# Kernel tuning notes

Measured on AMD Instinct MI355X. Metric: run time of the kernel, lower is better.

## Reference

```python
import jax, jax.numpy as jnp
import numpy as np

# --- static config (from init_kwargs) ---
B = 256        # num graphs
NPG = 128      # nodes per graph
EPG = 512      # edges per graph
DIN = 128      # dim_node
D = 256        # dim_hidden
RATIO = 0.5    # causal_ratio
N_RES = int(RATIO * EPG)
BN_EPS = 1e-5


def setup_inputs() -> dict:
    key = jax.random.key(0)
    ks = jax.random.split(key, 24)
    N = B * NPG
    x = jax.random.normal(ks[0], (N, DIN), jnp.float32)
    # edges confined within each graph, contiguous per graph (graph-sorted)
    src = jax.random.randint(ks[1], (B, EPG), 0, NPG)
    dst = jax.random.randint(ks[2], (B, EPG), 0, NPG)
    off = (jnp.arange(B, dtype=jnp.int32) * NPG)[:, None]
    edge_index = jnp.stack([(src + off).reshape(-1), (dst + off).reshape(-1)], 0).astype(jnp.int32)
    batch = jnp.repeat(jnp.arange(B, dtype=jnp.int32), NPG)

    s = 0.05
    def rn(k, shape):
        return jax.random.normal(k, shape, jnp.float32) * s
    p = dict(
        x=x, edge_index=edge_index, batch=batch,
        vemb=rn(ks[3], (1, D)),
        # conv1 GIN mlp: Linear(DIN,2D) -> BN -> ReLU -> Linear(2D,D)
        W1a=rn(ks[4], (DIN, 2 * D)), b1a=jnp.zeros((2 * D,)),
        g1a=jnp.ones((2 * D,)), be1a=jnp.zeros((2 * D,)),
        W1b=rn(ks[5], (2 * D, D)), b1b=jnp.zeros((D,)),
        g1=jnp.ones((D,)), be1=jnp.zeros((D,)),          # outer batch_norm1
        # conv2 GIN mlp
        W2a=rn(ks[6], (D, 2 * D)), b2a=jnp.zeros((2 * D,)),
        g2a=jnp.ones((2 * D,)), be2a=jnp.zeros((2 * D,)),
        W2b=rn(ks[7], (2 * D, D)), b2b=jnp.zeros((D,)),
        g2=jnp.ones((D,)), be2=jnp.zeros((D,)),          # outer batch_norm2
        # edge scorer: Linear(2D, 1)
        Wl=rn(ks[8], (2 * D, 1)), bl=jnp.zeros((1,)),
    )
    return p


def _bn(h, g, b):
    mu = h.mean(0)
    var = jnp.mean((h - mu) ** 2, 0)
    return (h - mu) * jax.lax.rsqrt(var + BN_EPS) * g + b


def reference(x, edge_index, batch, vemb,
              W1a, b1a, g1a, be1a, W1b, b1b, g1, be1,
              W2a, b2a, g2a, be2a, W2b, b2b, g2, be2,
              Wl, bl):
    N = x.shape[0]
    row, col = edge_index[0], edge_index[1]

    def gin(h, Wa, ba, ga, bta, Wb, bb):
        # GINConv, eps=0: mlp(h + sum_{j->i} h_j), aggregate src feats at dst
        agg = jax.ops.segment_sum(h[row], col, num_segments=N)
        z = (h + agg) @ Wa + ba
        z = jax.nn.relu(_bn(z, ga, bta))
        return z @ Wb + bb

    # layer 1: conv1 -> bn -> relu (dropout_rate = 0)
    post = jax.nn.relu(_bn(gin(x, W1a, b1a, g1a, be1a, W1b, b1b), g1, be1))
    # virtual node gather (embedding of index 0, one per graph)
    vfeat = jnp.broadcast_to(vemb[0], (B, D))
    post = post + vfeat[batch]
    # layer 2 (last): conv2 -> bn, no relu
    xn = _bn(gin(post, W2a, b2a, g2a, be2a, W2b, b2b), g2, be2)

    # edge scoring
    erep = jnp.concatenate([xn[row], xn[col]], axis=-1)          # [E, 2D]
    pred = (erep @ Wl + bl.astype(erep.dtype)).reshape(-1)       # [E]

    # per-graph top-k split (equal EPG edges per graph)
    pw = pred.reshape(B, EPG)
    order = jnp.argsort(-pw, axis=1)
    idx_r, idx_d = order[:, :N_RES], order[:, N_RES:]
    causal_w = jnp.take_along_axis(pw, idx_r, 1).reshape(-1)
    conf_w = -jnp.take_along_axis(pw, idx_d, 1).reshape(-1)
    ei = edge_index.reshape(2, B, EPG)
    causal_ei = jnp.take_along_axis(ei, jnp.broadcast_to(idx_r[None], (2, B, N_RES)), axis=2).reshape(2, -1)
    conf_ei = jnp.take_along_axis(ei, jnp.broadcast_to(idx_d[None], (2, B, EPG - N_RES)), axis=2).reshape(2, -1)
    return (causal_ei, causal_w, conf_ei, conf_w, pred)
```

## Files before the change

### kernel.cpp

```cpp
#include <hip/hip_runtime.h>

#define BGR   256
#define NPG   128
#define EPG   512
#define DIN   128
#define DD    256
#define DD2   512
#define NTOT  (BGR * NPG)
#define ETOT  (BGR * EPG)
#define NRES  (EPG / 2)
#define NCHUNK 256
#define MP    136

#define OFF_CEI  0
#define OFF_CW   (2 * BGR * NRES)
#define OFF_FEI  (OFF_CW + BGR * NRES)
#define OFF_FW   (OFF_FEI + 2 * BGR * NRES)
#define OFF_PRED (OFF_FW + BGR * NRES)

typedef unsigned short ushortt;
typedef __attribute__((ext_vector_type(4))) unsigned short us4;
typedef __attribute__((ext_vector_type(8))) unsigned short us8;
typedef __attribute__((ext_vector_type(8))) short short8;
typedef __attribute__((ext_vector_type(4))) float f32x4;

__device__ __forceinline__ ushortt f2bf(float f) {
    unsigned int u = __float_as_uint(f);
    unsigned int r = (u + 0x7fffu + ((u >> 16) & 1u)) >> 16;
    return (ushortt)r;
}
__device__ __forceinline__ float bf2f(ushortt u) {
    return __uint_as_float(((unsigned int)u) << 16);
}

__device__ __forceinline__ void g2lds16(const void* g, void* l) {
    __builtin_amdgcn_global_load_lds(
        (const __attribute__((address_space(1))) unsigned int*)g,
        (__attribute__((address_space(3))) unsigned int*)l, 16, 0, 0);
}

__global__ __launch_bounds__(256) void convert_all(const float* __restrict__ W1a,
                                                   const float* __restrict__ W1b,
                                                   const float* __restrict__ W2a,
                                                   const float* __restrict__ W2b,
                                                   ushortt* __restrict__ Wt1a,
                                                   ushortt* __restrict__ Wt1b,
                                                   ushortt* __restrict__ Wt2a,
                                                   ushortt* __restrict__ Wt2b) {
    const int idx = blockIdx.x * 256 + threadIdx.x;
    if (idx < 65536) {
        const int k = idx >> 9, n = idx & 511;
        Wt1a[n * DIN + k] = f2bf(W1a[idx]);
    } else if (idx < 196608) {
        const int i = idx - 65536;
        const int k = i >> 8, n = i & 255;
        Wt1b[n * DD2 + k] = f2bf(W1b[i]);
    } else if (idx < 327680) {
        const int i = idx - 196608;
        const int k = i >> 9, n = i & 511;
        Wt2a[n * DD + k] = f2bf(W2a[i]);
    } else if (idx < 458752) {
        const int i = idx - 327680;
        const int k = i >> 8, n = i & 255;
        Wt2b[n * DD2 + k] = f2bf(W2b[i]);
    }
}

__global__ __launch_bounds__(256) void build_adj(const int* __restrict__ ei,
                                                 ushortt* __restrict__ Madj) {
    __shared__ int cnt[NPG * NPG];
    const int b = blockIdx.x, t = threadIdx.x;
    for (int i = t; i < NPG * NPG; i += 256) cnt[i] = 0;
    __syncthreads();
    for (int e = t; e < EPG; e += 256) {
        const int src = ei[b * EPG + e] - b * NPG;
        const int dst = ei[ETOT + b * EPG + e] - b * NPG;
        atomicAdd(&cnt[dst * NPG + src], 1);
    }
    __syncthreads();
#pragma unroll
    for (int k = 0; k < 8; ++k) {
        const int i0 = (t + k * 256) * 8;
        us8 o;
#pragma unroll
        for (int e = 0; e < 8; ++e) {
            const int i = i0 + e;
            const int v = cnt[i] + (((i >> 7) == (i & 127)) ? 1 : 0);
            o[e] = f2bf((float)v);
        }
        *(us8*)&Madj[(size_t)b * NPG * NPG + i0] = o;
    }
}

__global__ __launch_bounds__(256) void agg1_mm(const float* __restrict__ x,
                                               const ushortt* __restrict__ Madj,
                                               ushortt* __restrict__ s1) {
    __shared__ ushortt Ms[NPG * MP];
    __shared__ ushortt XT[DIN * MP];
    const int b = blockIdx.x, t = threadIdx.x;
    const int wave = t >> 6, lane = t & 63;
    const int qd = lane >> 4, r = lane & 15;
    const ushortt* Mg = Madj + (size_t)b * NPG * NPG;
#pragma unroll
    for (int k = 0; k < 8; ++k) {
        const int ch = t + k * 256;
        const int m = ch >> 4, sc = (ch & 15) * 8;
        *(us8*)&Ms[m * MP + sc] = *(const us8*)&Mg[m * NPG + sc];
    }
#pragma unroll 4
    for (int it = 0; it < 64; ++it) {
        const int s = it * 2 + (t >> 7);
        const int c = t & 127;
        XT[c * MP + s] = f2bf(x[(size_t)(b * NPG + s) * DIN + c]);
    }
    __syncthreads();
    const int wm = (wave >> 1) * 64, wn = (wave & 1) * 64;
    f32x4 acc[4][4] = {};
#pragma unroll
    for (int ks = 0; ks < 4; ++ks) {
        const int k0 = ks * 32 + qd * 8;
        short8 af[4], bfr[4];
#pragma unroll
        for (int i = 0; i < 4; ++i)
            af[i] = *(const short8*)&Ms[(wm + i * 16 + r) * MP + k0];
#pragma unroll
        for (int j = 0; j < 4; ++j)
            bfr[j] = *(const short8*)&XT[(wn + j * 16 + r) * MP + k0];
#pragma unroll
        for (int i = 0; i < 4; ++i)
#pragma unroll
            for (int j = 0; j < 4; ++j)
                acc[i][j] = __builtin_amdgcn_mfma_f32_16x16x32_bf16(af[i], bfr[j], acc[i][j], 0, 0, 0);
    }
    __syncthreads();
    ushortt* Cs = Ms;
#pragma unroll
    for (int j = 0; j < 4; ++j) {
        const int coll = wn + j * 16 + r;
#pragma unroll
        for (int i = 0; i < 4; ++i)
#pragma unroll
            for (int tt = 0; tt < 4; ++tt)
                Cs[(wm + i * 16 + qd * 4 + tt) * DIN + coll] = f2bf(acc[i][j][tt]);
    }
    __syncthreads();
#pragma unroll
    for (int k = 0; k < 8; ++k) {
        const int ch = t + k * 256;
        const int row = ch >> 4, colc = (ch & 15) * 8;
        *(us8*)&s1[(size_t)(b * NPG + row) * DIN + colc] = *(const us8*)&Cs[row * DIN + colc];
    }
}

__global__ __launch_bounds__(256) void agg2_mm(const ushortt* __restrict__ h,
                                               const float* __restrict__ scale,
                                               const float* __restrict__ shift,
                                               const float* __restrict__ vemb,
                                               const ushortt* __restrict__ Madj,
                                               ushortt* __restrict__ s2) {
    __shared__ ushortt Ms[NPG * MP];
    __shared__ ushortt PT[NPG * MP];
    const int nb = blockIdx.x, b = blockIdx.y, t = threadIdx.x;
    const int wave = t >> 6, lane = t & 63;
    const int qd = lane >> 4, r = lane & 15;
    const ushortt* Mg = Madj + (size_t)b * NPG * NPG;
#pragma unroll
    for (int k = 0; k < 8; ++k) {
        const int ch = t + k * 256;
        const int m = ch >> 4, sc = (ch & 15) * 8;
        *(us8*)&Ms[m * MP + sc] = *(const us8*)&Mg[m * NPG + sc];
    }
    const int cl = t & 127;
    const int c = nb * 128 + cl;
    const float scv = scale[c], shv = shift[c], vev = vemb[c];
#pragma unroll 4
    for (int it = 0; it < 64; ++it) {
        const int s = it * 2 + (t >> 7);
        float v = fmaf(bf2f(h[(size_t)(b * NPG + s) * DD + c]), scv, shv);
        PT[cl * MP + s] = f2bf(fmaxf(v, 0.0f) + vev);
    }
    __syncthreads();
    const int wm = (wave >> 1) * 64, wn = (wave & 1) * 64;
    f32x4 acc[4][4] = {};
#pragma unroll
    for (int ks = 0; ks < 4; ++ks) {
        const int k0 = ks * 32 + qd * 8;
        short8 af[4], bfr[4];
#pragma unroll
        for (int i = 0; i < 4; ++i)
            af[i] = *(const short8*)&Ms[(wm + i * 16 + r) * MP + k0];
#pragma unroll
        for (int j = 0; j < 4; ++j)
            bfr[j] = *(const short8*)&PT[(wn + j * 16 + r) * MP + k0];
#pragma unroll
        for (int i = 0; i < 4; ++i)
#pragma unroll
            for (int j = 0; j < 4; ++j)
                acc[i][j] = __builtin_amdgcn_mfma_f32_16x16x32_bf16(af[i], bfr[j], acc[i][j], 0, 0, 0);
    }
    __syncthreads();
    ushortt* Cs = Ms;
#pragma unroll
    for (int j = 0; j < 4; ++j) {
        const int coll = wn + j * 16 + r;
#pragma unroll
        for (int i = 0; i < 4; ++i)
#pragma unroll
            for (int tt = 0; tt < 4; ++tt)
                Cs[(wm + i * 16 + qd * 4 + tt) * 128 + coll] = f2bf(acc[i][j][tt]);
    }
    __syncthreads();
#pragma unroll
    for (int k = 0; k < 8; ++k) {
        const int ch = t + k * 256;
        const int row = ch >> 4, colc = (ch & 15) * 8;
        *(us8*)&s2[(size_t)(b * NPG + row) * DD + nb * 128 + colc] =
            *(const us8*)&Cs[row * 128 + colc];
    }
}

#define BM 128
#define BN 128
#define BK 32
__global__ __launch_bounds__(256) void gemm_mfma(const ushortt* __restrict__ A,
                                                 const ushortt* __restrict__ Wt,
                                                 const float* __restrict__ bias,
                                                 ushortt* __restrict__ C,
                                                 float* __restrict__ psum,
                                                 float* __restrict__ psumsq,
                                                 int M, int N, int K) {
    __shared__ ushortt As[BM * BK];
    __shared__ ushortt Bs[BN * BK];
    __shared__ ushortt Cs[BM * BN];
    __shared__ float redS[2][BN];
    __shared__ float redQ[2][BN];
    const int tid  = threadIdx.x;
    const int wave = tid >> 6;
    const int lane = tid & 63;
    const int qd = lane >> 4;
    const int r  = lane & 15;
    const int wm = (wave >> 1) * 64;
    const int wn = (wave & 1) * 64;
    const int m0 = blockIdx.y * BM;
    const int n0 = blockIdx.x * BN;

    f32x4 acc[4][4] = {};

    for (int k0 = 0; k0 < K; k0 += BK) {
#pragma unroll
        for (int s = 0; s < 2; ++s) {
            const int o   = wave * 128 + s * 64 + lane;
            const int row = o >> 2;
            const int cg  = o & 3;
            g2lds16(A  + (size_t)(m0 + row) * K + k0 + cg * 8,
                    &As[(size_t)(wave * 128 + s * 64) * 8]);
            g2lds16(Wt + (size_t)(n0 + row) * K + k0 + cg * 8,
                    &Bs[(size_t)(wave * 128 + s * 64) * 8]);
        }
        __syncthreads();
        short8 af[4], bfr[4];
#pragma unroll
        for (int i = 0; i < 4; ++i)
            af[i] = *(const short8*)&As[(wm + i * 16 + r) * BK + qd * 8];
#pragma unroll
        for (int j = 0; j < 4; ++j)
            bfr[j] = *(const short8*)&Bs[(wn + j * 16 + r) * BK + qd * 8];
#pragma unroll
        for (int i = 0; i < 4; ++i)
#pragma unroll
            for (int j = 0; j < 4; ++j)
                acc[i][j] = __builtin_amdgcn_mfma_f32_16x16x32_bf16(af[i], bfr[j], acc[i][j], 0, 0, 0);
        __syncthreads();
    }

#pragma unroll
    for (int j = 0; j < 4; ++j) {
        const int coll = wn + j * 16 + r;
        const float bv = bias[n0 + coll];
        float s = 0.0f, q = 0.0f;
#pragma unroll
        for (int i = 0; i < 4; ++i) {
#pragma unroll
            for (int t = 0; t < 4; ++t) {
                const float v = acc[i][j][t] + bv;
                Cs[(wm + i * 16 + qd * 4 + t) * BN + coll] = f2bf(v);
                s += v;
                q = fmaf(v, v, q);
            }
        }
        s += __shfl_xor(s, 16); s += __shfl_xor(s, 32);
        q += __shfl_xor(q, 16); q += __shfl_xor(q, 32);
        if (qd == 0) {
            redS[wave >> 1][coll] = s;
            redQ[wave >> 1][coll] = q;
        }
    }
    __syncthreads();
    if (tid < BN) {
        psum[(size_t)blockIdx.y * N + n0 + tid]   = redS[0][tid] + redS[1][tid];
        psumsq[(size_t)blockIdx.y * N + n0 + tid] = redQ[0][tid] + redQ[1][tid];
    }
#pragma unroll
    for (int s8 = 0; s8 < 8; ++s8) {
        const int c    = tid + 256 * s8;
        const int row  = c >> 4;
        const int colc = (c & 15) * 8;
        const us8 v = *(const us8*)&Cs[row * BN + colc];
        *(us8*)&C[(size_t)(m0 + row) * N + n0 + colc] = v;
    }
}

__global__ __launch_bounds__(256) void bn_finalize(const float* __restrict__ psum,
                                                   const float* __restrict__ psumsq,
                                                   const float* __restrict__ g,
                                                   const float* __restrict__ be,
                                                   int ncols,
                                                   float* __restrict__ scale,
                                                   float* __restrict__ shift) {
    const int c = blockIdx.x * 256 + threadIdx.x;
    double s = 0.0, s2 = 0.0;
    for (int k = 0; k < NCHUNK; ++k) {
        s += (double)psum[(size_t)k * ncols + c];
        s2 += (double)psumsq[(size_t)k * ncols + c];
    }
    const double mean = s / (double)NTOT;
    const double var = s2 / (double)NTOT - mean * mean;
    const double rs = 1.0 / sqrt(var + 1e-5);
    const float sc = (float)((double)g[c] * rs);
    scale[c] = sc;
    shift[c] = (float)((double)be[c] - mean * (double)sc);
}

__global__ __launch_bounds__(256) void bn_apply_vec(const ushortt* __restrict__ z,
                                                    const float* __restrict__ scale,
                                                    const float* __restrict__ shift,
                                                    ushortt* __restrict__ outp,
                                                    int ncolmask) {
    const size_t gi = (size_t)blockIdx.x * 256 + threadIdx.x;
    const size_t base = gi * 8;
    const int c0 = (int)(base & (size_t)ncolmask);
    const us8 z8 = *(const us8*)&z[base];
    us8 o;
#pragma unroll
    for (int e = 0; e < 8; ++e) {
        float v = fmaf(bf2f(z8[e]), scale[c0 + e], shift[c0 + e]);
        v = fmaxf(v, 0.0f);
        o[e] = f2bf(v);
    }
    *(us8*)&outp[base] = o;
}

__global__ __launch_bounds__(256) void node_dots_bn(const ushortt* __restrict__ h2,
                                                    const float* __restrict__ scale,
                                                    const float* __restrict__ shift,
                                                    const float* __restrict__ Wl,
                                                    float* __restrict__ pa,
                                                    float* __restrict__ pb) {
    const int wave = threadIdx.x >> 6;
    const int lane = threadIdx.x & 63;
    const int node = blockIdx.x * 4 + wave;
    const us4 z4 = *(const us4*)&h2[(size_t)node * DD + lane * 4];
    const float4 sc = *(const float4*)&scale[lane * 4];
    const float4 sh = *(const float4*)&shift[lane * 4];
    const float4 w0 = *(const float4*)&Wl[lane * 4];
    const float4 w1 = *(const float4*)&Wl[DD + lane * 4];
    const float x0 = fmaf(bf2f(z4.x), sc.x, sh.x);
    const float x1 = fmaf(bf2f(z4.y), sc.y, sh.y);
    const float x2 = fmaf(bf2f(z4.z), sc.z, sh.z);
    const float x3 = fmaf(bf2f(z4.w), sc.w, sh.w);
    float sa = x0 * w0.x + x1 * w0.y + x2 * w0.z + x3 * w0.w;
    float sb = x0 * w1.x + x1 * w1.y + x2 * w1.z + x3 * w1.w;
#pragma unroll
    for (int off = 32; off >= 1; off >>= 1) {
        sa += __shfl_down(sa, off);
        sb += __shfl_down(sb, off);
    }
    if (lane == 0) {
        pa[node] = sa;
        pb[node] = sb;
    }
}

__global__ __launch_bounds__(EPG) void sort_write(const float* __restrict__ pa,
                                                  const float* __restrict__ pb,
                                                  const float* __restrict__ bl,
                                                  const int* __restrict__ ei,
                                                  float* __restrict__ out) {
    __shared__ float pw[EPG];
    __shared__ int ord[EPG];
    const int b = blockIdx.x;
    const int t = threadIdx.x;
    const int rg = ei[b * EPG + t];
    const int cg = ei[ETOT + b * EPG + t];
    const float v = pa[rg] + pb[cg] + bl[0];
    pw[t] = v;
    out[OFF_PRED + b * EPG + t] = v;
    __syncthreads();
    int rank = 0;
#pragma unroll 8
    for (int k = 0; k < EPG; ++k) {
        const float u = pw[k];
        rank += (u > v) || (u == v && k < t);
    }
    ord[rank] = t;
    __syncthreads();
    const int j = ord[t];
    const float wv = pw[j];
    const float e0 = (float)ei[b * EPG + j];
    const float e1 = (float)ei[ETOT + b * EPG + j];
    if (t < NRES) {
        out[OFF_CEI + b * NRES + t] = e0;
        out[OFF_CEI + BGR * NRES + b * NRES + t] = e1;
        out[OFF_CW + b * NRES + t] = wv;
    } else {
        const int p = t - NRES;
        out[OFF_FEI + b * NRES + p] = e0;
        out[OFF_FEI + BGR * NRES + b * NRES + p] = e1;
        out[OFF_FW + b * NRES + p] = -wv;
    }
}

extern "C" void kernel_launch(void* const* d_in, const int* in_sizes, int n_in,
                              void* d_out, int out_size, void* d_ws, size_t ws_size,
                              hipStream_t stream) {
    (void)in_sizes; (void)n_in; (void)out_size; (void)ws_size;
    const float* x    = (const float*)d_in[0];
    const int*   ei   = (const int*)d_in[1];
    const float* vemb = (const float*)d_in[3];
    const float* W1a  = (const float*)d_in[4];
    const float* b1a  = (const float*)d_in[5];
    const float* g1a  = (const float*)d_in[6];
    const float* be1a = (const float*)d_in[7];
    const float* W1b  = (const float*)d_in[8];
    const float* b1b  = (const float*)d_in[9];
    const float* g1   = (const float*)d_in[10];
    const float* be1  = (const float*)d_in[11];
    const float* W2a  = (const float*)d_in[12];
    const float* b2a  = (const float*)d_in[13];
    const float* g2a  = (const float*)d_in[14];
    const float* be2a = (const float*)d_in[15];
    const float* W2b  = (const float*)d_in[16];
    const float* b2b  = (const float*)d_in[17];
    const float* g2   = (const float*)d_in[18];
    const float* be2  = (const float*)d_in[19];
    const float* Wl   = (const float*)d_in[20];
    const float* bl   = (const float*)d_in[21];
    float* out = (float*)d_out;

    char* wp = (char*)d_ws;
    auto alloc = [&](size_t bytes) -> char* {
        char* r = wp;
        wp += (bytes + 255) & ~(size_t)255;
        return r;
    };
    ushortt* zb    = (ushortt*)alloc((size_t)NTOT * 512 * 2);
    ushortt* bufC  = (ushortt*)alloc((size_t)NTOT * 512 * 2);
    ushortt* bufD  = (ushortt*)alloc((size_t)NTOT * 256 * 2);
    ushortt* bufS1 = (ushortt*)alloc((size_t)NTOT * 128 * 2);
    ushortt* Madj  = (ushortt*)alloc((size_t)BGR * NPG * NPG * 2);
    ushortt* Wt1a  = (ushortt*)alloc((size_t)DIN * DD2 * 2);
    ushortt* Wt1b  = (ushortt*)alloc((size_t)DD2 * DD * 2);
    ushortt* Wt2a  = (ushortt*)alloc((size_t)DD * DD2 * 2);
    ushortt* Wt2b  = (ushortt*)alloc((size_t)DD2 * DD * 2);
    float*   psum   = (float*)alloc((size_t)NCHUNK * 512 * 4);
    float*   psumsq = (float*)alloc((size_t)NCHUNK * 512 * 4);
    float*   scale  = (float*)alloc(512 * 4);
    float*   shift  = (float*)alloc(512 * 4);
    float*   pa     = (float*)alloc((size_t)NTOT * 4);
    float*   pb     = (float*)alloc((size_t)NTOT * 4);

    convert_all<<<1792, 256, 0, stream>>>(W1a, W1b, W2a, W2b, Wt1a, Wt1b, Wt2a, Wt2b);

    build_adj<<<BGR, 256, 0, stream>>>(ei, Madj);

    agg1_mm<<<BGR, 256, 0, stream>>>(x, Madj, bufS1);

    gemm_mfma<<<dim3(DD2 / BN, NTOT / BM), 256, 0, stream>>>(bufS1, Wt1a, b1a, zb, psum, psumsq, NTOT, DD2, DIN);
    bn_finalize<<<2, 256, 0, stream>>>(psum, psumsq, g1a, be1a, DD2, scale, shift);
    bn_apply_vec<<<(NTOT * DD2) / 2048, 256, 0, stream>>>(zb, scale, shift, bufC, DD2 - 1);

    gemm_mfma<<<dim3(DD / BN, NTOT / BM), 256, 0, stream>>>(bufC, Wt1b, b1b, zb, psum, psumsq, NTOT, DD, DD2);
    bn_finalize<<<1, 256, 0, stream>>>(psum, psumsq, g1, be1, DD, scale, shift);

    agg2_mm<<<dim3(2, BGR), 256, 0, stream>>>(zb, scale, shift, vemb, Madj, bufD);

    gemm_mfma<<<dim3(DD2 / BN, NTOT / BM), 256, 0, stream>>>(bufD, Wt2a, b2a, zb, psum, psumsq, NTOT, DD2, DD);
    bn_finalize<<<2, 256, 0, stream>>>(psum, psumsq, g2a, be2a, DD2, scale, shift);
    bn_apply_vec<<<(NTOT * DD2) / 2048, 256, 0, stream>>>(zb, scale, shift, bufC, DD2 - 1);

    gemm_mfma<<<dim3(DD / BN, NTOT / BM), 256, 0, stream>>>(bufC, Wt2b, b2b, zb, psum, psumsq, NTOT, DD, DD2);
    bn_finalize<<<1, 256, 0, stream>>>(psum, psumsq, g2, be2, DD, scale, shift);

    node_dots_bn<<<NTOT / 4, 256, 0, stream>>>(zb, scale, shift, Wl, pa, pb);

    sort_write<<<BGR, EPG, 0, stream>>>(pa, pb, bl, ei, out);
}
```

Measured before the change: 344.7 us.

## Fuse whole GIN pipeline into one cooperative persistent kernel with grid syncs

Replaces the sequence of many separate launches (weight convert, adjacency build, aggregations, four GEMMs, BN finalize/apply, dots, sort) with a single cooperative kernel of one 512-thread block per graph, keeping per-graph adjacency and hidden activations resident in about 146 KB of LDS and separating BN statistic phases with grid.sync. The aim is to remove launch overhead and the global round trips for intermediates like bufC, bufS1 and Madj. In exchange it depends on all 256 blocks being co-resident, adds many grid-wide barriers, and runs each GEMM as per-graph tiles that reload weights in every block.

After: 538.7 us. 56.3% more time.

```diff
diff --git a/kernel.cpp b/kernel.cpp
--- a/kernel.cpp
+++ b/kernel.cpp
@@ -1,4 +1,7 @@
 #include <hip/hip_runtime.h>
+#include <hip/hip_cooperative_groups.h>
+
+namespace cg = cooperative_groups;
 
 #define BGR   256
 #define NPG   128
@@ -9,8 +12,13 @@
 #define NTOT  (BGR * NPG)
 #define ETOT  (BGR * EPG)
 #define NRES  (EPG / 2)
-#define NCHUNK 256
 #define MP    136
+
+#define SM_A  0
+#define SM_H  34816
+#define SM_B  104448
+#define SM_S  141312
+#define SM_TOTAL 149504
 
 #define OFF_CEI  0
 #define OFF_CW   (2 * BGR * NRES)
@@ -19,7 +27,6 @@
 #define OFF_PRED (OFF_FW + BGR * NRES)
 
 typedef unsigned short ushortt;
-typedef __attribute__((ext_vector_type(4))) unsigned short us4;
 typedef __attribute__((ext_vector_type(8))) unsigned short us8;
 typedef __attribute__((ext_vector_type(8))) short short8;
 typedef __attribute__((ext_vector_type(4))) float f32x4;
@@ -32,391 +39,417 @@
 __device__ __forceinline__ float bf2f(ushortt u) {
     return __uint_as_float(((unsigned int)u) << 16);
 }
-
 __device__ __forceinline__ void g2lds16(const void* g, void* l) {
     __builtin_amdgcn_global_load_lds(
         (const __attribute__((address_space(1))) unsigned int*)g,
         (__attribute__((address_space(3))) unsigned int*)l, 16, 0, 0);
 }
 
-__global__ __launch_bounds__(256) void convert_all(const float* __restrict__ W1a,
-                                                   const float* __restrict__ W1b,
-                                                   const float* __restrict__ W2a,
-                                                   const float* __restrict__ W2b,
-                                                   ushortt* __restrict__ Wt1a,
-                                                   ushortt* __restrict__ Wt1b,
-                                                   ushortt* __restrict__ Wt2a,
-                                                   ushortt* __restrict__ Wt2b) {
-    const int idx = blockIdx.x * 256 + threadIdx.x;
-    if (idx < 65536) {
-        const int k = idx >> 9, n = idx & 511;
-        Wt1a[n * DIN + k] = f2bf(W1a[idx]);
-    } else if (idx < 196608) {
-        const int i = idx - 65536;
-        const int k = i >> 8, n = i & 255;
-        Wt1b[n * DD2 + k] = f2bf(W1b[i]);
-    } else if (idx < 327680) {
-        const int i = idx - 196608;
-        const int k = i >> 9, n = i & 511;
-        Wt2a[n * DD + k] = f2bf(W2a[i]);
-    } else if (idx < 458752) {
-        const int i = idx - 327680;
-        const int k = i >> 8, n = i & 255;
-        Wt2b[n * DD2 + k] = f2bf(W2b[i]);
-    }
-}
-
-__global__ __launch_bounds__(256) void build_adj(const int* __restrict__ ei,
-                                                 ushortt* __restrict__ Madj) {
-    __shared__ int cnt[NPG * NPG];
-    const int b = blockIdx.x, t = threadIdx.x;
-    for (int i = t; i < NPG * NPG; i += 256) cnt[i] = 0;
-    __syncthreads();
-    for (int e = t; e < EPG; e += 256) {
-        const int src = ei[b * EPG + e] - b * NPG;
-        const int dst = ei[ETOT + b * EPG + e] - b * NPG;
-        atomicAdd(&cnt[dst * NPG + src], 1);
-    }
-    __syncthreads();
-#pragma unroll
-    for (int k = 0; k < 8; ++k) {
-        const int i0 = (t + k * 256) * 8;
-        us8 o;
-#pragma unroll
-        for (int e = 0; e < 8; ++e) {
-            const int i = i0 + e;
-            const int v = cnt[i] + (((i >> 7) == (i & 127)) ? 1 : 0);
-            o[e] = f2bf((float)v);
-        }
-        *(us8*)&Madj[(size_t)b * NPG * NPG + i0] = o;
-    }
-}
-
-__global__ __launch_bounds__(256) void agg1_mm(const float* __restrict__ x,
-                                               const ushortt* __restrict__ Madj,
-                                               ushortt* __restrict__ s1) {
-    __shared__ ushortt Ms[NPG * MP];
-    __shared__ ushortt XT[DIN * MP];
-    const int b = blockIdx.x, t = threadIdx.x;
+__device__ __forceinline__ void mfma_tile_ld(const ushortt* Ap, const ushortt* Bp,
+                                             int wm, int wn, int qd, int r,
+                                             f32x4 acc[4][2]) {
+#pragma unroll
+    for (int ks = 0; ks < 4; ++ks) {
+        const int k0 = ks * 32 + qd * 8;
+        short8 af[4], bfr[2];
+#pragma unroll
+        for (int i = 0; i < 4; ++i)
+            af[i] = *(const short8*)&Ap[(wm + i * 16 + r) * MP + k0];
+#pragma unroll
+        for (int j = 0; j < 2; ++j)
+            bfr[j] = *(const short8*)&Bp[(wn + j * 16 + r) * MP + k0];
+#pragma unroll
+        for (int i = 0; i < 4; ++i)
+#pragma unroll
+            for (int j = 0; j < 2; ++j)
+                acc[i][j] = __builtin_amdgcn_mfma_f32_16x16x32_bf16(af[i], bfr[j], acc[i][j], 0, 0, 0);
+    }
+}
+
+__device__ __forceinline__ void scatter_rowmajor(ushortt* dst, f32x4 acc[4][2],
+                                                 int wm, int wn, int qd, int r) {
+#pragma unroll
+    for (int j = 0; j < 2; ++j) {
+        const int col = wn + j * 16 + r;
+#pragma unroll
+        for (int i = 0; i < 4; ++i)
+#pragma unroll
+            for (int tt = 0; tt < 4; ++tt)
+                dst[(wm + i * 16 + qd * 4 + tt) * MP + col] = f2bf(acc[i][j][tt]);
+    }
+}
+
+__device__ __forceinline__ void zgemm_phase(char* smem, int b, int t,
+                                            const ushortt* __restrict__ Wt, int wtStride, int khn,
+                                            const float* __restrict__ bias,
+                                            ushortt* __restrict__ zb,
+                                            float* __restrict__ psA, float* __restrict__ pqA) {
     const int wave = t >> 6, lane = t & 63;
     const int qd = lane >> 4, r = lane & 15;
-    const ushortt* Mg = Madj + (size_t)b * NPG * NPG;
-#pragma unroll
-    for (int k = 0; k < 8; ++k) {
-        const int ch = t + k * 256;
-        const int m = ch >> 4, sc = (ch & 15) * 8;
-        *(us8*)&Ms[m * MP + sc] = *(const us8*)&Mg[m * NPG + sc];
-    }
-#pragma unroll 4
-    for (int it = 0; it < 64; ++it) {
-        const int s = it * 2 + (t >> 7);
-        const int c = t & 127;
-        XT[c * MP + s] = f2bf(x[(size_t)(b * NPG + s) * DIN + c]);
-    }
-    __syncthreads();
-    const int wm = (wave >> 1) * 64, wn = (wave & 1) * 64;
-    f32x4 acc[4][4] = {};
-#pragma unroll
-    for (int ks = 0; ks < 4; ++ks) {
-        const int k0 = ks * 32 + qd * 8;
-        short8 af[4], bfr[4];
-#pragma unroll
-        for (int i = 0; i < 4; ++i)
-            af[i] = *(const short8*)&Ms[(wm + i * 16 + r) * MP + k0];
-#pragma unroll
-        for (int j = 0; j < 4; ++j)
-            bfr[j] = *(const short8*)&XT[(wn + j * 16 + r) * MP + k0];
-#pragma unroll
-        for (int i = 0; i < 4; ++i)
-#pragma unroll
-            for (int j = 0; j < 4; ++j)
-                acc[i][j] = __builtin_amdgcn_mfma_f32_16x16x32_bf16(af[i], bfr[j], acc[i][j], 0, 0, 0);
-    }
-    __syncthreads();
-    ushortt* Cs = Ms;
-#pragma unroll
-    for (int j = 0; j < 4; ++j) {
-        const int coll = wn + j * 16 + r;
-#pragma unroll
-        for (int i = 0; i < 4; ++i)
-#pragma unroll
-            for (int tt = 0; tt < 4; ++tt)
-                Cs[(wm + i * 16 + qd * 4 + tt) * DIN + coll] = f2bf(acc[i][j][tt]);
-    }
-    __syncthreads();
-#pragma unroll
-    for (int k = 0; k < 8; ++k) {
-        const int ch = t + k * 256;
-        const int row = ch >> 4, colc = (ch & 15) * 8;
-        *(us8*)&s1[(size_t)(b * NPG + row) * DIN + colc] = *(const us8*)&Cs[row * DIN + colc];
-    }
-}
-
-__global__ __launch_bounds__(256) void agg2_mm(const ushortt* __restrict__ h,
-                                               const float* __restrict__ scale,
-                                               const float* __restrict__ shift,
-                                               const float* __restrict__ vemb,
-                                               const ushortt* __restrict__ Madj,
-                                               ushortt* __restrict__ s2) {
-    __shared__ ushortt Ms[NPG * MP];
-    __shared__ ushortt PT[NPG * MP];
-    const int nb = blockIdx.x, b = blockIdx.y, t = threadIdx.x;
+    const int wm = (wave >> 2) * 64, wn = (wave & 3) * 32;
+    ushortt* Wc = (ushortt*)(smem + SM_B);
+    float* redS = (float*)(smem + SM_S + 4096);
+    float* redQ = (float*)(smem + SM_S + 5120);
+    for (int nc = 0; nc < 4; ++nc) {
+        f32x4 acc[4][2] = {};
+        for (int kh = 0; kh < khn; ++kh) {
+#pragma unroll
+            for (int kk = 0; kk < 4; ++kk) {
+                const int ch = t + kk * 512;
+                const int n = ch >> 4, k8 = (ch & 15) * 8;
+                *(us8*)&Wc[n * MP + k8] =
+                    *(const us8*)&Wt[(size_t)(nc * 128 + n) * wtStride + kh * 128 + k8];
+            }
+            __syncthreads();
+            const ushortt* Ap = (const ushortt*)(smem + SM_H) + kh * 17408;
+            mfma_tile_ld(Ap, Wc, wm, wn, qd, r, acc);
+            __syncthreads();
+        }
+        ushortt* Cs = Wc;
+#pragma unroll
+        for (int j = 0; j < 2; ++j) {
+            const int coll = wn + j * 16 + r;
+            const float bv = bias[nc * 128 + coll];
+            float s = 0.f, q = 0.f;
+#pragma unroll
+            for (int i = 0; i < 4; ++i)
+#pragma unroll
+                for (int tt = 0; tt < 4; ++tt) {
+                    const float v = acc[i][j][tt] + bv;
+                    Cs[(wm + i * 16 + qd * 4 + tt) * MP + coll] = f2bf(v);
+                    s += v; q = fmaf(v, v, q);
+                }
+            s += __shfl_xor(s, 16); s += __shfl_xor(s, 32);
+            q += __shfl_xor(q, 16); q += __shfl_xor(q, 32);
+            if (qd == 0) { redS[(wm >> 6) * 128 + coll] = s; redQ[(wm >> 6) * 128 + coll] = q; }
+        }
+        __syncthreads();
+        if (t < 128) {
+            psA[(size_t)b * DD2 + nc * 128 + t] = redS[t] + redS[128 + t];
+            pqA[(size_t)b * DD2 + nc * 128 + t] = redQ[t] + redQ[128 + t];
+        }
+#pragma unroll
+        for (int kk = 0; kk < 4; ++kk) {
+            const int ch = t + kk * 512;
+            const int row = ch >> 4, colc = (ch & 15) * 8;
+            *(us8*)&zb[(size_t)(b * NPG + row) * DD2 + nc * 128 + colc] =
+                *(const us8*)&Cs[row * MP + colc];
+        }
+        __syncthreads();
+    }
+}
+
+__device__ __forceinline__ void hgemm_phase(char* smem, int b, int t,
+                                            const ushortt* __restrict__ zglob,
+                                            const ushortt* __restrict__ Wt,
+                                            const float* __restrict__ scAg,
+                                            const float* __restrict__ shAg,
+                                            const float* __restrict__ bias,
+                                            float* __restrict__ psB, float* __restrict__ pqB) {
     const int wave = t >> 6, lane = t & 63;
     const int qd = lane >> 4, r = lane & 15;
-    const ushortt* Mg = Madj + (size_t)b * NPG * NPG;
-#pragma unroll
-    for (int k = 0; k < 8; ++k) {
-        const int ch = t + k * 256;
-        const int m = ch >> 4, sc = (ch & 15) * 8;
-        *(us8*)&Ms[m * MP + sc] = *(const us8*)&Mg[m * NPG + sc];
-    }
-    const int cl = t & 127;
-    const int c = nb * 128 + cl;
-    const float scv = scale[c], shv = shift[c], vev = vemb[c];
-#pragma unroll 4
-    for (int it = 0; it < 64; ++it) {
-        const int s = it * 2 + (t >> 7);
-        float v = fmaf(bf2f(h[(size_t)(b * NPG + s) * DD + c]), scv, shv);
-        PT[cl * MP + s] = f2bf(fmaxf(v, 0.0f) + vev);
-    }
+    const int wm = (wave >> 2) * 64, wn = (wave & 3) * 32;
+    float* scs = (float*)(smem + SM_S);
+    float* shs = scs + 512;
+    float* redS = (float*)(smem + SM_S + 4096);
+    float* redQ = (float*)(smem + SM_S + 5120);
+    ushortt* As = (ushortt*)(smem + SM_B);
+    ushortt* Bs = As + 4096;
+    ushortt* hT = (ushortt*)(smem + SM_H);
+    scs[t] = scAg[t]; shs[t] = shAg[t];
     __syncthreads();
-    const int wm = (wave >> 1) * 64, wn = (wave & 1) * 64;
-    f32x4 acc[4][4] = {};
-#pragma unroll
-    for (int ks = 0; ks < 4; ++ks) {
-        const int k0 = ks * 32 + qd * 8;
-        short8 af[4], bfr[4];
-#pragma unroll
-        for (int i = 0; i < 4; ++i)
-            af[i] = *(const short8*)&Ms[(wm + i * 16 + r) * MP + k0];
-#pragma unroll
-        for (int j = 0; j < 4; ++j)
-            bfr[j] = *(const short8*)&PT[(wn + j * 16 + r) * MP + k0];
-#pragma unroll
-        for (int i = 0; i < 4; ++i)
-#pragma unroll
-            for (int j = 0; j < 4; ++j)
-                acc[i][j] = __builtin_amdgcn_mfma_f32_16x16x32_bf16(af[i], bfr[j], acc[i][j], 0, 0, 0);
-    }
-    __syncthreads();
-    ushortt* Cs = Ms;
-#pragma unroll
-    for (int j = 0; j < 4; ++j) {
-        const int coll = wn + j * 16 + r;
-#pragma unroll
-        for (int i = 0; i < 4; ++i)
-#pragma unroll
-            for (int tt = 0; tt < 4; ++tt)
-                Cs[(wm + i * 16 + qd * 4 + tt) * 128 + coll] = f2bf(acc[i][j][tt]);
-    }
-    __syncthreads();
-#pragma unroll
-    for (int k = 0; k < 8; ++k) {
-        const int ch = t + k * 256;
-        const int row = ch >> 4, colc = (ch & 15) * 8;
-        *(us8*)&s2[(size_t)(b * NPG + row) * DD + nb * 128 + colc] =
-            *(const us8*)&Cs[row * 128 + colc];
-    }
-}
-
-#define BM 128
-#define BN 128
-#define BK 32
-__global__ __launch_bounds__(256) void gemm_mfma(const ushortt* __restrict__ A,
-                                                 const ushortt* __restrict__ Wt,
-                                                 const float* __restrict__ bias,
-                                                 ushortt* __restrict__ C,
-                                                 float* __restrict__ psum,
-                                                 float* __restrict__ psumsq,
-                                                 int M, int N, int K) {
-    __shared__ ushortt As[BM * BK];
-    __shared__ ushortt Bs[BN * BK];
-    __shared__ ushortt Cs[BM * BN];
-    __shared__ float redS[2][BN];
-    __shared__ float redQ[2][BN];
-    const int tid  = threadIdx.x;
-    const int wave = tid >> 6;
-    const int lane = tid & 63;
-    const int qd = lane >> 4;
-    const int r  = lane & 15;
-    const int wm = (wave >> 1) * 64;
-    const int wn = (wave & 1) * 64;
-    const int m0 = blockIdx.y * BM;
-    const int n0 = blockIdx.x * BN;
-
-    f32x4 acc[4][4] = {};
-
-    for (int k0 = 0; k0 < K; k0 += BK) {
-#pragma unroll
-        for (int s = 0; s < 2; ++s) {
-            const int o   = wave * 128 + s * 64 + lane;
-            const int row = o >> 2;
-            const int cg  = o & 3;
-            g2lds16(A  + (size_t)(m0 + row) * K + k0 + cg * 8,
-                    &As[(size_t)(wave * 128 + s * 64) * 8]);
-            g2lds16(Wt + (size_t)(n0 + row) * K + k0 + cg * 8,
-                    &Bs[(size_t)(wave * 128 + s * 64) * 8]);
-        }
-        __syncthreads();
-        short8 af[4], bfr[4];
-#pragma unroll
-        for (int i = 0; i < 4; ++i)
-            af[i] = *(const short8*)&As[(wm + i * 16 + r) * BK + qd * 8];
-#pragma unroll
-        for (int j = 0; j < 4; ++j)
-            bfr[j] = *(const short8*)&Bs[(wn + j * 16 + r) * BK + qd * 8];
-#pragma unroll
-        for (int i = 0; i < 4; ++i)
-#pragma unroll
-            for (int j = 0; j < 4; ++j)
-                acc[i][j] = __builtin_amdgcn_mfma_f32_16x16x32_bf16(af[i], bfr[j], acc[i][j], 0, 0, 0);
-        __syncthreads();
-    }
-
-#pragma unroll
-    for (int j = 0; j < 4; ++j) {
-        const int coll = wn + j * 16 + r;
-        const float bv = bias[n0 + coll];
-        float s = 0.0f, q = 0.0f;
-#pragma unroll
-        for (int i = 0; i < 4; ++i) {
-#pragma unroll
-            for (int t = 0; t < 4; ++t) {
-                const float v = acc[i][j][t] + bv;
-                Cs[(wm + i * 16 + qd * 4 + t) * BN + coll] = f2bf(v);
-                s += v;
-                q = fmaf(v, v, q);
+    const int row = t >> 2, cg = t & 3;
+    for (int nc = 0; nc < 2; ++nc) {
+        f32x4 acc[4][2] = {};
+        for (int k0 = 0; k0 < DD2; k0 += 32) {
+            g2lds16(Wt + (size_t)(nc * 128 + row) * DD2 + k0 + cg * 8,
+                    &Bs[(size_t)(wave * 64) * 8]);
+            {
+                const us8 a8 = *(const us8*)&zglob[(size_t)(b * NPG + row) * DD2 + k0 + cg * 8];
+                const float4 s4a = *(const float4*)&scs[k0 + cg * 8];
+                const float4 s4b = *(const float4*)&scs[k0 + cg * 8 + 4];
+                const float4 h4a = *(const float4*)&shs[k0 + cg * 8];
+                const float4 h4b = *(const float4*)&shs[k0 + cg * 8 + 4];
+                us8 t8;
+                t8[0] = f2bf(fmaxf(fmaf(bf2f(a8[0]), s4a.x, h4a.x), 0.0f));
+                t8[1] = f2bf(fmaxf(fmaf(bf2f(a8[1]), s4a.y, h4a.y), 0.0f));
+                t8[2] = f2bf(fmaxf(fmaf(bf2f(a8[2]), s4a.z, h4a.z), 0.0f));
+                t8[3] = f2bf(fmaxf(fmaf(bf2f(a8[3]), s4a.w, h4a.w), 0.0f));
+                t8[4] = f2bf(fmaxf(fmaf(bf2f(a8[4]), s4b.x, h4b.x), 0.0f));
+                t8[5] = f2bf(fmaxf(fmaf(bf2f(a8[5]), s4b.y, h4b.y), 0.0f));
+                t8[6] = f2bf(fmaxf(fmaf(bf2f(a8[6]), s4b.z, h4b.z), 0.0f));
+                t8[7] = f2bf(fmaxf(fmaf(bf2f(a8[7]), s4b.w, h4b.w), 0.0f));
+                *(us8*)&As[row * 32 + cg * 8] = t8;
             }
-        }
-        s += __shfl_xor(s, 16); s += __shfl_xor(s, 32);
-        q += __shfl_xor(q, 16); q += __shfl_xor(q, 32);
-        if (qd == 0) {
-            redS[wave >> 1][coll] = s;
-            redQ[wave >> 1][coll] = q;
-        }
-    }
-    __syncthreads();
-    if (tid < BN) {
-        psum[(size_t)blockIdx.y * N + n0 + tid]   = redS[0][tid] + redS[1][tid];
-        psumsq[(size_t)blockIdx.y * N + n0 + tid] = redQ[0][tid] + redQ[1][tid];
-    }
-#pragma unroll
-    for (int s8 = 0; s8 < 8; ++s8) {
-        const int c    = tid + 256 * s8;
-        const int row  = c >> 4;
-        const int colc = (c & 15) * 8;
-        const us8 v = *(const us8*)&Cs[row * BN + colc];
-        *(us8*)&C[(size_t)(m0 + row) * N + n0 + colc] = v;
-    }
-}
-
-__global__ __launch_bounds__(256) void bn_finalize(const float* __restrict__ psum,
-                                                   const float* __restrict__ psumsq,
-                                                   const float* __restrict__ g,
-                                                   const float* __restrict__ be,
-                                                   int ncols,
-                                                   float* __restrict__ scale,
-                                                   float* __restrict__ shift) {
-    const int c = blockIdx.x * 256 + threadIdx.x;
-    double s = 0.0, s2 = 0.0;
-    for (int k = 0; k < NCHUNK; ++k) {
-        s += (double)psum[(size_t)k * ncols + c];
-        s2 += (double)psumsq[(size_t)k * ncols + c];
-    }
-    const double mean = s / (double)NTOT;
-    const double var = s2 / (double)NTOT - mean * mean;
-    const double rs = 1.0 / sqrt(var + 1e-5);
-    const float sc = (float)((double)g[c] * rs);
-    scale[c] = sc;
-    shift[c] = (float)((double)be[c] - mean * (double)sc);
-}
-
-__global__ __launch_bounds__(256) void bn_apply_vec(const ushortt* __restrict__ z,
-                                                    const float* __restrict__ scale,
-                                                    const float* __restrict__ shift,
-                                                    ushortt* __restrict__ outp,
-                                                    int ncolmask) {
-    const size_t gi = (size_t)blockIdx.x * 256 + threadIdx.x;
-    const size_t base = gi * 8;
-    const int c0 = (int)(base & (size_t)ncolmask);
-    const us8 z8 = *(const us8*)&z[base];
-    us8 o;
-#pragma unroll
-    for (int e = 0; e < 8; ++e) {
-        float v = fmaf(bf2f(z8[e]), scale[c0 + e], shift[c0 + e]);
-        v = fmaxf(v, 0.0f);
-        o[e] = f2bf(v);
-    }
-    *(us8*)&outp[base] = o;
-}
-
-__global__ __launch_bounds__(256) void node_dots_bn(const ushortt* __restrict__ h2,
-                                                    const float* __restrict__ scale,
-                                                    const float* __restrict__ shift,
-                                                    const float* __restrict__ Wl,
-                                                    float* __restrict__ pa,
-                                                    float* __restrict__ pb) {
-    const int wave = threadIdx.x >> 6;
-    const int lane = threadIdx.x & 63;
-    const int node = blockIdx.x * 4 + wave;
-    const us4 z4 = *(const us4*)&h2[(size_t)node * DD + lane * 4];
-    const float4 sc = *(const float4*)&scale[lane * 4];
-    const float4 sh = *(const float4*)&shift[lane * 4];
-    const float4 w0 = *(const float4*)&Wl[lane * 4];
-    const float4 w1 = *(const float4*)&Wl[DD + lane * 4];
-    const float x0 = fmaf(bf2f(z4.x), sc.x, sh.x);
-    const float x1 = fmaf(bf2f(z4.y), sc.y, sh.y);
-    const float x2 = fmaf(bf2f(z4.z), sc.z, sh.z);
-    const float x3 = fmaf(bf2f(z4.w), sc.w, sh.w);
-    float sa = x0 * w0.x + x1 * w0.y + x2 * w0.z + x3 * w0.w;
-    float sb = x0 * w1.x + x1 * w1.y + x2 * w1.z + x3 * w1.w;
-#pragma unroll
-    for (int off = 32; off >= 1; off >>= 1) {
-        sa += __shfl_down(sa, off);
-        sb += __shfl_down(sb, off);
-    }
-    if (lane == 0) {
-        pa[node] = sa;
-        pb[node] = sb;
-    }
-}
-
-__global__ __launch_bounds__(EPG) void sort_write(const float* __restrict__ pa,
-                                                  const float* __restrict__ pb,
-                                                  const float* __restrict__ bl,
-                                                  const int* __restrict__ ei,
-                                                  float* __restrict__ out) {
-    __shared__ float pw[EPG];
-    __shared__ int ord[EPG];
+            __syncthreads();
+            short8 af[4], bfr[2];
+            const int kq = qd * 8;
+#pragma unroll
+            for (int i = 0; i < 4; ++i)
+                af[i] = *(const short8*)&As[(wm + i * 16 + r) * 32 + kq];
+#pragma unroll
+            for (int j = 0; j < 2; ++j)
+                bfr[j] = *(const short8*)&Bs[(wn + j * 16 + r) * 32 + kq];
+#pragma unroll
+            for (int i = 0; i < 4; ++i)
+#pragma unroll
+                for (int j = 0; j < 2; ++j)
+                    acc[i][j] = __builtin_amdgcn_mfma_f32_16x16x32_bf16(af[i], bfr[j], acc[i][j], 0, 0, 0);
+            __syncthreads();
+        }
+#pragma unroll
+        for (int j = 0; j < 2; ++j) {
+            const int coll = wn + j * 16 + r;
+            const float bv = bias[nc * 128 + coll];
+            float s = 0.f, q = 0.f;
+#pragma unroll
+            for (int i = 0; i < 4; ++i)
+#pragma unroll
+                for (int tt = 0; tt < 4; ++tt) {
+                    const float v = acc[i][j][tt] + bv;
+                    hT[(nc * 128 + coll) * 136 + (wm + i * 16 + qd * 4 + tt)] = f2bf(v);
+                    s += v; q = fmaf(v, v, q);
+                }
+            s += __shfl_xor(s, 16); s += __shfl_xor(s, 32);
+            q += __shfl_xor(q, 16); q += __shfl_xor(q, 32);
+            if (qd == 0) { redS[(wm >> 6) * 128 + coll] = s; redQ[(wm >> 6) * 128 + coll] = q; }
+        }
+        __syncthreads();
+        if (t < 128) {
+            psB[(size_t)b * DD + nc * 128 + t] = redS[t] + redS[128 + t];
+            pqB[(size_t)b * DD + nc * 128 + t] = redQ[t] + redQ[128 + t];
+        }
+        __syncthreads();
+    }
+}
+
+__device__ __forceinline__ void finalize_cols(const float* __restrict__ ps,
+                                              const float* __restrict__ pq,
+                                              const float* __restrict__ g,
+                                              const float* __restrict__ be,
+                                              int ncols, int t,
+                                              float* __restrict__ scg,
+                                              float* __restrict__ shg) {
+    if (t < ncols) {
+        double s = 0.0, s2 = 0.0;
+        for (int k = 0; k < 256; ++k) {
+            s += (double)ps[(size_t)k * ncols + t];
+            s2 += (double)pq[(size_t)k * ncols + t];
+        }
+        const double mean = s / (double)NTOT;
+        const double var = s2 / (double)NTOT - mean * mean;
+        const double rs = 1.0 / sqrt(var + 1e-5);
+        const float sc = (float)((double)g[t] * rs);
+        scg[t] = sc;
+        shg[t] = (float)((double)be[t] - mean * (double)sc);
+    }
+}
+
+__global__ __launch_bounds__(512, 2) void mega(
+    const float* __restrict__ x, const int* __restrict__ ei,
+    const float* __restrict__ vemb,
+    const float* __restrict__ W1a, const float* __restrict__ b1a,
+    const float* __restrict__ g1a, const float* __restrict__ be1a,
+    const float* __restrict__ W1b, const float* __restrict__ b1b,
+    const float* __restrict__ g1, const float* __restrict__ be1,
+    const float* __restrict__ W2a, const float* __restrict__ b2a,
+    const float* __restrict__ g2a, const float* __restrict__ be2a,
+    const float* __restrict__ W2b, const float* __restrict__ b2b,
+    const float* __restrict__ g2, const float* __restrict__ be2,
+    const float* __restrict__ Wl, const float* __restrict__ bl,
+    ushortt* __restrict__ zb,
+    ushortt* __restrict__ Wt1a, ushortt* __restrict__ Wt1b,
+    ushortt* __restrict__ Wt2a, ushortt* __restrict__ Wt2b,
+    float* __restrict__ psA, float* __restrict__ pqA,
+    float* __restrict__ psB, float* __restrict__ pqB,
+    float* __restrict__ scAg, float* __restrict__ shAg,
+    float* __restrict__ scBg, float* __restrict__ shBg,
+    float* __restrict__ out) {
+    __shared__ __align__(16) char smem[SM_TOTAL];
+    cg::grid_group grid = cg::this_grid();
     const int b = blockIdx.x;
     const int t = threadIdx.x;
-    const int rg = ei[b * EPG + t];
-    const int cg = ei[ETOT + b * EPG + t];
-    const float v = pa[rg] + pb[cg] + bl[0];
-    pw[t] = v;
-    out[OFF_PRED + b * EPG + t] = v;
-    __syncthreads();
-    int rank = 0;
+    const int wave = t >> 6, lane = t & 63;
+    const int qd = lane >> 4, r = lane & 15;
+    const int wm = (wave >> 2) * 64, wn = (wave & 3) * 32;
+
+    if (b < 112) {
+        const float* W; ushortt* Wt; int Nsrc, Ktot, kr0, nc0;
+        if (b < 16)      { W = W1a; Wt = Wt1a; Nsrc = 512; Ktot = 128; kr0 = (b >> 3) * 64; nc0 = (b & 7) * 64; }
+        else if (b < 48) { const int i = b - 16; W = W1b; Wt = Wt1b; Nsrc = 256; Ktot = 512; kr0 = (i >> 2) * 64; nc0 = (i & 3) * 64; }
+        else if (b < 80) { const int i = b - 48; W = W2a; Wt = Wt2a; Nsrc = 512; Ktot = 256; kr0 = (i >> 3) * 64; nc0 = (i & 7) * 64; }
+        else             { const int i = b - 80; W = W2b; Wt = Wt2b; Nsrc = 256; Ktot = 512; kr0 = (i >> 2) * 64; nc0 = (i & 3) * 64; }
+        ushortt* tile = (ushortt*)smem;
+#pragma unroll
+        for (int kk = 0; kk < 2; ++kk) {
+            const int idx = t + kk * 512;
+            const int rr = idx >> 4, c4 = (idx & 15) * 4;
+            const float4 v = *(const float4*)&W[(size_t)(kr0 + rr) * Nsrc + nc0 + c4];
+            tile[rr * 67 + c4 + 0] = f2bf(v.x);
+            tile[rr * 67 + c4 + 1] = f2bf(v.y);
+            tile[rr * 67 + c4 + 2] = f2bf(v.z);
+            tile[rr * 67 + c4 + 3] = f2bf(v.w);
+        }
+        __syncthreads();
+        {
+            const int n = t >> 3, k8 = (t & 7) * 8;
+            us8 o;
+#pragma unroll
+            for (int j = 0; j < 8; ++j) o[j] = tile[(k8 + j) * 67 + n];
+            *(us8*)&Wt[(size_t)(nc0 + n) * Ktot + kr0 + k8] = o;
+        }
+        __syncthreads();
+    }
+
+    {
+        int* cnt = (int*)(smem + SM_H);
+        ushortt* Ms = (ushortt*)(smem + SM_A);
+        ushortt* XT = (ushortt*)(smem + SM_B);
+        for (int i = t; i < NPG * NPG; i += 512) cnt[i] = 0;
+        __syncthreads();
+        {
+            const int src = ei[b * EPG + t] - b * NPG;
+            const int dst = ei[ETOT + b * EPG + t] - b * NPG;
+            atomicAdd(&cnt[dst * NPG + src], 1);
+        }
+        __syncthreads();
+#pragma unroll
+        for (int kk = 0; kk < 4; ++kk) {
+            const int ch = t + kk * 512;
+            const int m = ch >> 4, sc0 = (ch & 15) * 8;
+            us8 o;
+#pragma unroll
+            for (int e2 = 0; e2 < 8; ++e2)
+                o[e2] = f2bf((float)(cnt[m * NPG + sc0 + e2] + (m == sc0 + e2 ? 1 : 0)));
+            *(us8*)&Ms[m * MP + sc0] = o;
+        }
+#pragma unroll
+        for (int kk = 0; kk < 4; ++kk) {
+            const int ch = t + kk * 512;
+            const int c = ch & 127, s8 = ch >> 7;
+            us8 o;
+#pragma unroll
+            for (int j = 0; j < 8; ++j)
+                o[j] = f2bf(x[(size_t)(b * NPG + s8 * 8 + j) * DIN + c]);
+            *(us8*)&XT[c * MP + s8 * 8] = o;
+        }
+        __syncthreads();
+        f32x4 acc[4][2] = {};
+        mfma_tile_ld(Ms, XT, wm, wn, qd, r, acc);
+        __syncthreads();
+        scatter_rowmajor((ushortt*)(smem + SM_H), acc, wm, wn, qd, r);
+        __syncthreads();
+    }
+    grid.sync();
+
+    zgemm_phase(smem, b, t, Wt1a, DIN, 1, b1a, zb, psA, pqA);
+    grid.sync();
+    if (b == 0) finalize_cols(psA, pqA, g1a, be1a, DD2, t, scAg, shAg);
+    grid.sync();
+
+    hgemm_phase(smem, b, t, zb, Wt1b, scAg, shAg, b1b, psB, pqB);
+    grid.sync();
+    if (b == 0) finalize_cols(psB, pqB, g1, be1, DD, t, scBg, shBg);
+    grid.sync();
+
+    {
+        float* scs = (float*)(smem + SM_S);
+        float* shs = scs + 512;
+        if (t < DD) { scs[t] = scBg[t]; shs[t] = shBg[t]; }
+        __syncthreads();
+        ushortt* hT = (ushortt*)(smem + SM_H);
+#pragma unroll
+        for (int kk = 0; kk < 8; ++kk) {
+            const int ch = t + kk * 512;
+            const int c = ch >> 4, s8 = (ch & 15) * 8;
+            const us8 v = *(const us8*)&hT[c * 136 + s8];
+            const float scv = scs[c], shv = shs[c], vev = vemb[c];
+            us8 o;
+#pragma unroll
+            for (int j = 0; j < 8; ++j)
+                o[j] = f2bf(fmaxf(fmaf(bf2f(v[j]), scv, shv), 0.0f) + vev);
+            *(us8*)&hT[c * 136 + s8] = o;
+        }
+        __syncthreads();
+        const ushortt* Ms = (const ushortt*)(smem + SM_A);
+        for (int h = 0; h < 2; ++h) {
+            f32x4 acc[4][2] = {};
+            mfma_tile_ld(Ms, hT + h * 17408, wm, wn, qd, r, acc);
+            __syncthreads();
+            scatter_rowmajor((ushortt*)(smem + SM_H) + h * 17408, acc, wm, wn, qd, r);
+            __syncthreads();
+        }
+    }
+
+    zgemm_phase(smem, b, t, Wt2a, DD, 2, b2a, zb, psA, pqA);
+    grid.sync();
+    if (b == 0) finalize_cols(psA, pqA, g2a, be2a, DD2, t, scAg, shAg);
+    grid.sync();
+
+    hgemm_phase(smem, b, t, zb, Wt2b, scAg, shAg, b2b, psB, pqB);
+    grid.sync();
+    if (b == 0) finalize_cols(psB, pqB, g2, be2, DD, t, scBg, shBg);
+    grid.sync();
+
+    {
+        float* scs = (float*)(smem + SM_S);
+        float* shs = scs + 512;
+        if (t < DD) { scs[t] = scBg[t]; shs[t] = shBg[t]; }
+        __syncthreads();
+        const ushortt* hT = (const ushortt*)(smem + SM_H);
+        float* part  = (float*)(smem + SM_B);
+        float* partb = part + 512;
+        {
+            const int node = lane + (wave & 1) * 64;
+            const int cb = (wave >> 1) * 64;
+            float sa = 0.f, sb = 0.f;
+            for (int cc = 0; cc < 64; ++cc) {
+                const int c = cb + cc;
+                const float xv = fmaf(bf2f(hT[c * 136 + node]), scs[c], shs[c]);
+                sa = fmaf(xv, Wl[c], sa);
+                sb = fmaf(xv, Wl[DD + c], sb);
+            }
+            part[(wave >> 1) * 128 + node] = sa;
+            partb[(wave >> 1) * 128 + node] = sb;
+        }
+        __syncthreads();
+        float* pa = (float*)(smem + SM_S + 6144);
+        float* pb = pa + 128;
+        if (t < 128) {
+            pa[t] = part[t] + part[128 + t] + part[256 + t] + part[384 + t];
+            pb[t] = partb[t] + partb[128 + t] + partb[256 + t] + partb[384 + t];
+        }
+        __syncthreads();
+        float* pw = (float*)(smem + SM_B);
+        int* ord = (int*)(smem + SM_B + 2048);
+        const int rl = ei[b * EPG + t] - b * NPG;
+        const int cl = ei[ETOT + b * EPG + t] - b * NPG;
+        const float v = pa[rl] + pb[cl] + bl[0];
+        pw[t] = v;
+        out[OFF_PRED + b * EPG + t] = v;
+        __syncthreads();
+        int rank = 0;
 #pragma unroll 8
-    for (int k = 0; k < EPG; ++k) {
-        const float u = pw[k];
-        rank += (u > v) || (u == v && k < t);
-    }
-    ord[rank] = t;
-    __syncthreads();
-    const int j = ord[t];
-    const float wv = pw[j];
-    const float e0 = (float)ei[b * EPG + j];
-    const float e1 = (float)ei[ETOT + b * EPG + j];
-    if (t < NRES) {
-        out[OFF_CEI + b * NRES + t] = e0;
-        out[OFF_CEI + BGR * NRES + b * NRES + t] = e1;
-        out[OFF_CW + b * NRES + t] = wv;
-    } else {
-        const int p = t - NRES;
-        out[OFF_FEI + b * NRES + p] = e0;
-        out[OFF_FEI + BGR * NRES + b * NRES + p] = e1;
-        out[OFF_FW + b * NRES + p] = -wv;
+        for (int k = 0; k < EPG; ++k) {
+            const float u = pw[k];
+            rank += (u > v) || (u == v && k < t);
+        }
+        ord[rank] = t;
+        __syncthreads();
+        const int j = ord[t];
+        const float wv = pw[j];
+        const float e0 = (float)ei[b * EPG + j];
+        const float e1 = (float)ei[ETOT + b * EPG + j];
+        if (t < NRES) {
+            out[OFF_CEI + b * NRES + t] = e0;
+            out[OFF_CEI + BGR * NRES + b * NRES + t] = e1;
+            out[OFF_CW + b * NRES + t] = wv;
+        } else {
+            const int p = t - NRES;
+            out[OFF_FEI + b * NRES + p] = e0;
+            out[OFF_FEI + BGR * NRES + b * NRES + p] = e1;
+            out[OFF_FW + b * NRES + p] = -wv;
+        }
     }
 }
 
@@ -453,45 +486,32 @@
         wp += (bytes + 255) & ~(size_t)255;
         return r;
     };
-    ushortt* zb    = (ushortt*)alloc((size_t)NTOT * 512 * 2);
-    ushortt* bufC  = (ushortt*)alloc((size_t)NTOT * 512 * 2);
-    ushortt* bufD  = (ushortt*)alloc((size_t)NTOT * 256 * 2);
-    ushortt* bufS1 = (ushortt*)alloc((size_t)NTOT * 128 * 2);
-    ushortt* Madj  = (ushortt*)alloc((size_t)BGR * NPG * NPG * 2);
-    ushortt* Wt1a  = (ushortt*)alloc((size_t)DIN * DD2 * 2);
-    ushortt* Wt1b  = (ushortt*)alloc((size_t)DD2 * DD * 2);
-    ushortt* Wt2a  = (ushortt*)alloc((size_t)DD * DD2 * 2);
-    ushortt* Wt2b  = (ushortt*)alloc((size_t)DD2 * DD * 2);
-    float*   psum   = (float*)alloc((size_t)NCHUNK * 512 * 4);
-    float*   psumsq = (float*)alloc((size_t)NCHUNK * 512 * 4);
-    float*   scale  = (float*)alloc(512 * 4);
-    float*   shift  = (float*)alloc(512 * 4);
-    float*   pa     = (float*)alloc((size_t)NTOT * 4);
-    float*   pb     = (float*)alloc((size_t)NTOT * 4);
-
-    convert_all<<<1792, 256, 0, stream>>>(W1a, W1b, W2a, W2b, Wt1a, Wt1b, Wt2a, Wt2b);
-
-    build_adj<<<BGR, 256, 0, stream>>>(ei, Madj);
-
-    agg1_mm<<<BGR, 256, 0, stream>>>(x, Madj, bufS1);
-
-    gemm_mfma<<<dim3(DD2 / BN, NTOT / BM), 256, 0, stream>>>(bufS1, Wt1a, b1a, zb, psum, psumsq, NTOT, DD2, DIN);
-    bn_finalize<<<2, 256, 0, stream>>>(psum, psumsq, g1a, be1a, DD2, scale, shift);
-    bn_apply_vec<<<(NTOT * DD2) / 2048, 256, 0, stream>>>(zb, scale, shift, bufC, DD2 - 1);
-
-    gemm_mfma<<<dim3(DD / BN, NTOT / BM), 256, 0, stream>>>(bufC, Wt1b, b1b, zb, psum, psumsq, NTOT, DD, DD2);
-    bn_finalize<<<1, 256, 0, stream>>>(psum, psumsq, g1, be1, DD, scale, shift);
-
-    agg2_mm<<<dim3(2, BGR), 256, 0, stream>>>(zb, scale, shift, vemb, Madj, bufD);
-
-    gemm_mfma<<<dim3(DD2 / BN, NTOT / BM), 256, 0, stream>>>(bufD, Wt2a, b2a, zb, psum, psumsq, NTOT, DD2, DD);
-    bn_finalize<<<2, 256, 0, stream>>>(psum, psumsq, g2a, be2a, DD2, scale, shift);
-    bn_apply_vec<<<(NTOT * DD2) / 2048, 256, 0, stream>>>(zb, scale, shift, bufC, DD2 - 1);
-
-    gemm_mfma<<<dim3(DD / BN, NTOT / BM), 256, 0, stream>>>(bufC, Wt2b, b2b, zb, psum, psumsq, NTOT, DD, DD2);
-    bn_finalize<<<1, 256, 0, stream>>>(psum, psumsq, g2, be2, DD, scale, shift);
-
-    node_dots_bn<<<NTOT / 4, 256, 0, stream>>>(zb, scale, shift, Wl, pa, pb);
-
-    sort_write<<<BGR, EPG, 0, stream>>>(pa, pb, bl, ei, out);
-}
+    ushortt* zb   = (ushortt*)alloc((size_t)NTOT * DD2 * 2);
+    ushortt* Wt1a = (ushortt*)alloc((size_t)DIN * DD2 * 2);
+    ushortt* Wt1b = (ushortt*)alloc((size_t)DD2 * DD * 2);
+    ushortt* Wt2a = (ushortt*)alloc((size_t)DD * DD2 * 2);
+    ushortt* Wt2b = (ushortt*)alloc((size_t)DD2 * DD * 2);
+    float* psA = (float*)alloc((size_t)256 * DD2 * 4);
+    float* pqA = (float*)alloc((size_t)256 * DD2 * 4);
+    float* psB = (float*)alloc((size_t)256 * DD * 4);
+    float* pqB = (float*)alloc((size_t)256 * DD * 4);
+    float* scAg = (float*)alloc(DD2 * 4);
+    float* shAg = (float*)alloc(DD2 * 4);
+    float* scBg = (float*)alloc(DD * 4);
+    float* shBg = (float*)alloc(DD * 4);
+
+    void* kargs[] = {
+        (void*)&x, (void*)&ei, (void*)&vemb,
+        (void*)&W1a, (void*)&b1a, (void*)&g1a, (void*)&be1a,
+        (void*)&W1b, (void*)&b1b, (void*)&g1, (void*)&be1,
+        (void*)&W2a, (void*)&b2a, (void*)&g2a, (void*)&be2a,
+        (void*)&W2b, (void*)&b2b, (void*)&g2, (void*)&be2,
+        (void*)&Wl, (void*)&bl,
+        (void*)&zb, (void*)&Wt1a, (void*)&Wt1b, (void*)&Wt2a, (void*)&Wt2b,
+        (void*)&psA, (void*)&pqA, (void*)&psB, (void*)&pqB,
+        (void*)&scAg, (void*)&shAg, (void*)&scBg, (void*)&shBg,
+        (void*)&out
+    };
+    hipLaunchCooperativeKernel((const void*)mega, dim3(BGR), dim3(512),
+                               kargs, 0, stream);
+}
```
